# Kernel tuning notes

Measured on AMD Instinct MI355X. Metric: run time of the kernel, lower is better.

## Reference

```python
import jax, jax.numpy as jnp
import numpy as np

B, F_IN, F_OUT, D, K = 32, 64, 64, 512, 64


def setup_inputs() -> dict:
    key = jax.random.key(0)
    k1, k2, k3 = jax.random.split(key, 3)
    x = jax.random.normal(k1, (B, F_IN, D), dtype=jnp.float32)
    # Evaluated monomial-word operators: K matrices of size D x D
    word_ops = jax.random.normal(k2, (K, D, D), dtype=jnp.float32)
    # nn.init.uniform_ -> U[0,1)
    coeff = jax.random.uniform(k3, (F_OUT, F_IN, K), dtype=jnp.float32)
    return {"x": x, "word_ops": word_ops, "coeff": coeff}


def reference(x, word_ops, coeff):
    # Per sample in the torch code:
    #   evals[i, d, k] = (X @ W_k)[i, d] = sum_e X[i, e] * W[k, e, d]
    #   res = tensordot(coeff, evals, ([1, 2], [0, 2]))  -> [F_out, D]
    # Fully batched fused contraction (replaces the Python loop over batch):
    # evals: [B, F_in, D, K]
    evals = jnp.einsum('bie,ked->bidk', x, word_ops)
    # out: [B, F_out, D]
    out = jnp.einsum('oik,bidk->bod', coeff, evals)
    return out
```

## Files before the change

kernel.cpp:

```cpp
#include <hip/hip_runtime.h>


#define KK 32768

typedef __attribute__((ext_vector_type(8))) short bf16x8;
typedef __attribute__((ext_vector_type(4))) float f32x4;

__device__ __forceinline__ unsigned short f2bf(float f) {
  unsigned int u = __float_as_uint(f);
  return (unsigned short)((u + 0x7FFFu + ((u >> 16) & 1u)) >> 16);
}

__device__ __forceinline__ void gld16(void* lds, const void* g) {
  __builtin_amdgcn_global_load_lds((const __attribute__((address_space(1))) void*)g,
                                   (__attribute__((address_space(3))) void*)lds,
                                   16, 0, 0);
}

__global__ __launch_bounds__(256) void convW(const float* __restrict__ W,
                                             unsigned short* __restrict__ WbT) {
  __shared__ float tile[64][65];
  int bx = blockIdx.x;
  int k = bx >> 6, et = (bx >> 3) & 7, dt = bx & 7;
  int t = threadIdx.x;
  const float* src = W + ((size_t)k * 512 + (size_t)et * 64) * 512 + dt * 64;
  int rr = t >> 6, cc = t & 63;
#pragma unroll
  for (int p = 0; p < 16; p++) {
    int e = p * 4 + rr;
    tile[e][cc] = src[(size_t)e * 512 + cc];
  }
  __syncthreads();
  int dl = t >> 4, eg = t & 15;
#pragma unroll
  for (int p = 0; p < 4; p++) {
    int d = p * 16 + dl;
    ushort4 v;
    v.x = f2bf(tile[eg * 4 + 0][d]);
    v.y = f2bf(tile[eg * 4 + 1][d]);
    v.z = f2bf(tile[eg * 4 + 2][d]);
    v.w = f2bf(tile[eg * 4 + 3][d]);
    *(ushort4*)(WbT + (size_t)(dt * 64 + d) * KK + k * 512 + et * 64 + eg * 4) = v;
  }
}

__global__ __launch_bounds__(256) void convX(const float* __restrict__ x,
                                             unsigned short* __restrict__ xT) {
  int tid = blockIdx.x * 256 + threadIdx.x;
  int b = tid >> 15;
  int r = tid & 32767;
  int e = r >> 6, i = r & 63;
  xT[tid] = f2bf(x[((size_t)(b * 64 + i)) * 512 + e]);
}

__global__ __launch_bounds__(256) void convC(const float* __restrict__ c,
                                             unsigned short* __restrict__ cb) {
  int tid = blockIdx.x * 256 + threadIdx.x;
  int k = tid >> 12, r = tid & 4095;
  cb[tid] = f2bf(c[(size_t)r * 64 + k]);
}

__global__ __launch_bounds__(256) void tkern(const unsigned short* __restrict__ xT,
                                             const unsigned short* __restrict__ cb,
                                             unsigned short* __restrict__ Tb) {
  __shared__ unsigned short xe[128 * 88];
  __shared__ unsigned short ck[64 * 64];
  __shared__ unsigned short ot[64 * 136];
  int bx = blockIdx.x;
  int b = bx >> 8, k = (bx >> 2) & 63, eq = bx & 3;
  int t = threadIdx.x;
  {
    const bf16x8* src = (const bf16x8*)(xT + (size_t)b * 32768 + (size_t)eq * 128 * 64);
#pragma unroll
    for (int j = 0; j < 4; j++) {
      int idx = j * 256 + t, e = idx >> 3, c = idx & 7;
      *(bf16x8*)(xe + e * 88 + c * 8) = src[idx];
    }
    const bf16x8* cs = (const bf16x8*)(cb + (size_t)k * 4096);
#pragma unroll
    for (int j = 0; j < 2; j++) *(bf16x8*)(ck + (j * 256 + t) * 8) = cs[j * 256 + t];
  }
  __syncthreads();
  int wid = t >> 6, lane = t & 63, q = lane >> 4, l16 = lane & 15;
  int o0 = wid * 16;
  bf16x8 a0 = *(const bf16x8*)(ck + (o0 + l16) * 64 + q * 8);
  bf16x8 a1 = *(const bf16x8*)(ck + (o0 + l16) * 64 + q * 8 + 32);
#pragma unroll
  for (int et = 0; et < 8; et++) {
    int e = et * 16 + l16;
    bf16x8 b0 = *(const bf16x8*)(xe + e * 88 + q * 8);
    bf16x8 b1 = *(const bf16x8*)(xe + e * 88 + q * 8 + 32);
    f32x4 acc = {0.f, 0.f, 0.f, 0.f};
    acc = __builtin_amdgcn_mfma_f32_16x16x32_bf16(a0, b0, acc, 0, 0, 0);
    acc = __builtin_amdgcn_mfma_f32_16x16x32_bf16(a1, b1, acc, 0, 0, 0);
#pragma unroll
    for (int r2 = 0; r2 < 4; r2++)
      ot[(o0 + q * 4 + r2) * 136 + et * 16 + l16] = f2bf(acc[r2]);
  }
  __syncthreads();
  size_t base = ((size_t)(b * 64)) * KK + k * 512 + eq * 128;
#pragma unroll
  for (int j = 0; j < 4; j++) {
    int idx = j * 256 + t, o = idx >> 4, c = idx & 15;
    *(bf16x8*)(Tb + base + (size_t)o * KK + c * 8) = *(const bf16x8*)(ot + o * 136 + c * 8);
  }
}

__global__ __launch_bounds__(256, 4) void gemm_kern(const unsigned short* __restrict__ A,
                                                    const unsigned short* __restrict__ Bt,
                                                    float* __restrict__ out) {
  __shared__ unsigned short As[128 * 64];
  __shared__ unsigned short Bs[128 * 64];
  int bx = blockIdx.x;
  int ks = bx & 15, nt = (bx >> 4) & 3, mt = bx >> 6;
  int m0 = mt * 128, n0 = nt * 128, k0 = ks * 2048;
  int t = threadIdx.x;
  int wid = t >> 6, lane = t & 63, q = lane >> 4, l16 = lane & 15;
  int wm = (wid & 1) * 64, wn = (wid >> 1) * 64;
  f32x4 acc[4][4] = {};
  int srow = t >> 3;
  int cg = (t & 7) ^ (srow & 7);
  const char* gabase = (const char*)(A + (size_t)m0 * KK + k0) + (size_t)srow * 65536 + cg * 16;
  const char* gbbase = (const char*)(Bt + (size_t)n0 * KK + k0) + (size_t)srow * 65536 + cg * 16;
  int sw0 = q ^ (l16 & 7);
  int sw1 = (4 | q) ^ (l16 & 7);
#pragma unroll 1
  for (int kc = 0; kc < 2048; kc += 64) {
    const char* ga = gabase + (size_t)kc * 2;
    const char* gb = gbbase + (size_t)kc * 2;
#pragma unroll
    for (int j = 0; j < 4; j++) {
      gld16((char*)As + (j * 256 + t) * 16, ga + (size_t)j * 32 * 65536);
      gld16((char*)Bs + (j * 256 + t) * 16, gb + (size_t)j * 32 * 65536);
    }
    __syncthreads();
#pragma unroll
    for (int ks2 = 0; ks2 < 2; ks2++) {
      int slot = ks2 ? sw1 : sw0;
      bf16x8 af[4], bfr[4];
#pragma unroll
      for (int fr = 0; fr < 4; fr++)
        af[fr] = *(const bf16x8*)(As + (wm + fr * 16 + l16) * 64 + slot * 8);
#pragma unroll
      for (int fc = 0; fc < 4; fc++)
        bfr[fc] = *(const bf16x8*)(Bs + (wn + fc * 16 + l16) * 64 + slot * 8);
#pragma unroll
      for (int fr = 0; fr < 4; fr++)
#pragma unroll
        for (int fc = 0; fc < 4; fc++)
          acc[fr][fc] = __builtin_amdgcn_mfma_f32_16x16x32_bf16(af[fr], bfr[fc], acc[fr][fc], 0, 0, 0);
    }
    __syncthreads();
  }
#pragma unroll
  for (int fr = 0; fr < 4; fr++)
#pragma unroll
    for (int fc = 0; fc < 4; fc++)
#pragma unroll
      for (int r = 0; r < 4; r++)
        atomicAdd(&out[(size_t)(m0 + wm + fr * 16 + q * 4 + r) * 512 + n0 + wn + fc * 16 + l16],
                  acc[fr][fc][r]);
}

__global__ __launch_bounds__(256) void fallback_kern(const float* __restrict__ x,
                                                     const float* __restrict__ W,
                                                     const float* __restrict__ coeff,
                                                     float* __restrict__ out) {
  __shared__ float ev[64][129];
  int b = blockIdx.x >> 6, k = blockIdx.x & 63;
  int t = threadIdx.x, dl = t & 127, half = t >> 7;
  const float* xb = x + (size_t)b * 64 * 512;
  const float* Wk = W + (size_t)k * 512 * 512;
  for (int dc = 0; dc < 4; dc++) {
    int d = dc * 128 + dl;
    for (int i = half * 32; i < half * 32 + 32; i++) {
      float acc = 0.f;
      const float* xr = xb + (size_t)i * 512;
#pragma unroll 4
      for (int e = 0; e < 512; e++) acc += xr[e] * Wk[(size_t)e * 512 + d];
      ev[i][dl] = acc;
    }
    __syncthreads();
    for (int o = half * 32; o < half * 32 + 32; o++) {
      float s = 0.f;
#pragma unroll 8
      for (int i = 0; i < 64; i++) s += coeff[((size_t)o * 64 + i) * 64 + k] * ev[i][dl];
      atomicAdd(&out[((size_t)(b * 64 + o)) * 512 + d], s);
    }
    __syncthreads();
  }
}

extern "C" void kernel_launch(void* const* d_in, const int* in_sizes, int n_in,
                              void* d_out, int out_size, void* d_ws, size_t ws_size,
                              hipStream_t stream) {
  const float* x = (const float*)d_in[0];
  const float* W = (const float*)d_in[1];
  const float* coeff = (const float*)d_in[2];
  float* out = (float*)d_out;
  const size_t OFF_XT = 33554432;
  const size_t OFF_CB = OFF_XT + 2097152;
  const size_t OFF_TB = OFF_CB + 524288;
  const size_t NEED = OFF_TB + 134217728;

  hipMemsetAsync(d_out, 0, (size_t)out_size * sizeof(float), stream);
  if (ws_size >= NEED) {
    unsigned short* WbT = (unsigned short*)d_ws;
    unsigned short* xT  = (unsigned short*)((char*)d_ws + OFF_XT);
    unsigned short* cb  = (unsigned short*)((char*)d_ws + OFF_CB);
    unsigned short* Tb  = (unsigned short*)((char*)d_ws + OFF_TB);
    convW<<<4096, 256, 0, stream>>>(W, WbT);
    convX<<<4096, 256, 0, stream>>>(x, xT);
    convC<<<1024, 256, 0, stream>>>(coeff, cb);
    tkern<<<8192, 256, 0, stream>>>(xT, cb, Tb);
    gemm_kern<<<1024, 256, 0, stream>>>(Tb, WbT, out);
  } else {
    fallback_kern<<<2048, 256, 0, stream>>>(x, W, coeff, out);
  }
}
```

Measured before the change: 251.9 us.

## Retile GEMM with double-buffered LDS, enlarge tkern tiles, coalesce conversion kernels

The main GEMM moves to 256x128 tiles with a K-step of 32 and double-buffered LDS loads via global_load_lds. The next chunk is prefetched while the current one runs on MFMA, which aims to overlap memory with compute and halve the number of blocks doing atomics. tkern now computes a 64x256 tile per block using async LDS loads with XOR swizzling, so it reuses the coefficient fragments across more MFMAs. convX and convC become LDS-transposed, coalesced kernels. The costs are higher register pressure (occupancy bound of 2) and more LDS per block.

```diff
diff --git a/kernel.cpp b/kernel.cpp
--- a/kernel.cpp
+++ b/kernel.cpp
@@ -46,120 +46,178 @@
 
 __global__ __launch_bounds__(256) void convX(const float* __restrict__ x,
                                              unsigned short* __restrict__ xT) {
-  int tid = blockIdx.x * 256 + threadIdx.x;
-  int b = tid >> 15;
-  int r = tid & 32767;
-  int e = r >> 6, i = r & 63;
-  xT[tid] = f2bf(x[((size_t)(b * 64 + i)) * 512 + e]);
+  __shared__ unsigned short lds[64 * 130];
+  int bx = blockIdx.x;
+  int b = bx >> 2, ec = bx & 3;
+  int t = threadIdx.x;
+  const float* src = x + (size_t)b * 32768 + ec * 128;
+#pragma unroll
+  for (int j = 0; j < 32; j++) {
+    int idx = j * 256 + t;
+    int i = idx >> 7, e = idx & 127;
+    lds[i * 130 + e] = f2bf(src[(size_t)i * 512 + e]);
+  }
+  __syncthreads();
+  unsigned short* dst = xT + (size_t)b * 32768 + ec * 128 * 64;
+#pragma unroll
+  for (int j = 0; j < 32; j++) {
+    int idx = j * 256 + t;
+    int e = idx >> 6, i = idx & 63;
+    dst[idx] = lds[i * 130 + e];
+  }
 }
 
 __global__ __launch_bounds__(256) void convC(const float* __restrict__ c,
                                              unsigned short* __restrict__ cb) {
-  int tid = blockIdx.x * 256 + threadIdx.x;
-  int k = tid >> 12, r = tid & 4095;
-  cb[tid] = f2bf(c[(size_t)r * 64 + k]);
-}
-
-__global__ __launch_bounds__(256) void tkern(const unsigned short* __restrict__ xT,
-                                             const unsigned short* __restrict__ cb,
-                                             unsigned short* __restrict__ Tb) {
-  __shared__ unsigned short xe[128 * 88];
-  __shared__ unsigned short ck[64 * 64];
-  __shared__ unsigned short ot[64 * 136];
-  int bx = blockIdx.x;
-  int b = bx >> 8, k = (bx >> 2) & 63, eq = bx & 3;
-  int t = threadIdx.x;
+  __shared__ unsigned short lds[64 * 66];
+  int rb = blockIdx.x;
+  int t = threadIdx.x;
+  const float* src = c + (size_t)rb * 4096;
+#pragma unroll
+  for (int j = 0; j < 16; j++) {
+    int idx = j * 256 + t;
+    int r = idx >> 6, k = idx & 63;
+    lds[r * 66 + k] = f2bf(src[idx]);
+  }
+  __syncthreads();
+#pragma unroll
+  for (int j = 0; j < 16; j++) {
+    int idx = j * 256 + t;
+    int k = idx >> 6, r = idx & 63;
+    cb[(size_t)k * 4096 + rb * 64 + r] = lds[r * 66 + k];
+  }
+}
+
+__global__ __launch_bounds__(256, 2) void tkern(const unsigned short* __restrict__ xT,
+                                                const unsigned short* __restrict__ cb,
+                                                unsigned short* __restrict__ Tb) {
+  __shared__ char smem[40960];
+  unsigned short* xe = (unsigned short*)smem;
+  unsigned short* ck = (unsigned short*)(smem + 32768);
+  unsigned short* ot = (unsigned short*)smem;
+  int bx = blockIdx.x;
+  int eh = bx & 1, k = (bx >> 1) & 63, b = bx >> 7;
+  int t = threadIdx.x;
+  int srow = t >> 3, slot = t & 7;
+  int cg = slot ^ (srow & 7);
   {
-    const bf16x8* src = (const bf16x8*)(xT + (size_t)b * 32768 + (size_t)eq * 128 * 64);
-#pragma unroll
-    for (int j = 0; j < 4; j++) {
-      int idx = j * 256 + t, e = idx >> 3, c = idx & 7;
-      *(bf16x8*)(xe + e * 88 + c * 8) = src[idx];
-    }
-    const bf16x8* cs = (const bf16x8*)(cb + (size_t)k * 4096);
-#pragma unroll
-    for (int j = 0; j < 2; j++) *(bf16x8*)(ck + (j * 256 + t) * 8) = cs[j * 256 + t];
+    const unsigned short* gx = xT + (size_t)b * 32768 + (size_t)eh * 16384 + srow * 64 + cg * 8;
+#pragma unroll
+    for (int j = 0; j < 8; j++)
+      gld16((char*)xe + (j * 256 + t) * 16, gx + (size_t)j * 2048);
+    const unsigned short* gc = cb + (size_t)k * 4096 + srow * 64 + cg * 8;
+#pragma unroll
+    for (int j = 0; j < 2; j++)
+      gld16((char*)ck + (j * 256 + t) * 16, gc + (size_t)j * 2048);
   }
   __syncthreads();
   int wid = t >> 6, lane = t & 63, q = lane >> 4, l16 = lane & 15;
-  int o0 = wid * 16;
-  bf16x8 a0 = *(const bf16x8*)(ck + (o0 + l16) * 64 + q * 8);
-  bf16x8 a1 = *(const bf16x8*)(ck + (o0 + l16) * 64 + q * 8 + 32);
-#pragma unroll
-  for (int et = 0; et < 8; et++) {
-    int e = et * 16 + l16;
-    bf16x8 b0 = *(const bf16x8*)(xe + e * 88 + q * 8);
-    bf16x8 b1 = *(const bf16x8*)(xe + e * 88 + q * 8 + 32);
-    f32x4 acc = {0.f, 0.f, 0.f, 0.f};
-    acc = __builtin_amdgcn_mfma_f32_16x16x32_bf16(a0, b0, acc, 0, 0, 0);
-    acc = __builtin_amdgcn_mfma_f32_16x16x32_bf16(a1, b1, acc, 0, 0, 0);
-#pragma unroll
-    for (int r2 = 0; r2 < 4; r2++)
-      ot[(o0 + q * 4 + r2) * 136 + et * 16 + l16] = f2bf(acc[r2]);
-  }
-  __syncthreads();
-  size_t base = ((size_t)(b * 64)) * KK + k * 512 + eq * 128;
-#pragma unroll
-  for (int j = 0; j < 4; j++) {
-    int idx = j * 256 + t, o = idx >> 4, c = idx & 15;
-    *(bf16x8*)(Tb + base + (size_t)o * KK + c * 8) = *(const bf16x8*)(ot + o * 136 + c * 8);
-  }
-}
-
-__global__ __launch_bounds__(256, 4) void gemm_kern(const unsigned short* __restrict__ A,
+  f32x4 acc[4][4] = {};
+  bf16x8 af[4][2];
+#pragma unroll
+  for (int mf = 0; mf < 4; mf++)
+#pragma unroll
+    for (int ks2 = 0; ks2 < 2; ks2++) {
+      int row = mf * 16 + l16;
+      int s2 = (ks2 * 4 + q) ^ (row & 7);
+      af[mf][ks2] = *(const bf16x8*)(ck + row * 64 + s2 * 8);
+    }
+#pragma unroll
+  for (int nf = 0; nf < 4; nf++) {
+    int e = wid * 64 + nf * 16 + l16;
+#pragma unroll
+    for (int ks2 = 0; ks2 < 2; ks2++) {
+      int s2 = (ks2 * 4 + q) ^ (e & 7);
+      bf16x8 bfr = *(const bf16x8*)(xe + e * 64 + s2 * 8);
+#pragma unroll
+      for (int mf = 0; mf < 4; mf++)
+        acc[mf][nf] = __builtin_amdgcn_mfma_f32_16x16x32_bf16(af[mf][ks2], bfr, acc[mf][nf], 0, 0, 0);
+    }
+  }
+  __syncthreads();
+#pragma unroll
+  for (int mf = 0; mf < 4; mf++)
+#pragma unroll
+    for (int nf = 0; nf < 4; nf++)
+#pragma unroll
+      for (int r = 0; r < 4; r++) {
+        int o = mf * 16 + q * 4 + r;
+        int e = wid * 64 + nf * 16 + l16;
+        ot[o * 260 + e] = f2bf(acc[mf][nf][r]);
+      }
+  __syncthreads();
+  unsigned short* gdst = Tb + (size_t)(b * 64) * KK + (size_t)k * 512 + (size_t)eh * 256;
+#pragma unroll
+  for (int j = 0; j < 16; j++) {
+    int idx = j * 256 + t;
+    int o = idx >> 6, c = idx & 63;
+    *(ushort4*)(gdst + (size_t)o * KK + c * 4) = *(const ushort4*)(ot + o * 260 + c * 4);
+  }
+}
+
+__global__ __launch_bounds__(256, 2) void gemm_kern(const unsigned short* __restrict__ A,
                                                     const unsigned short* __restrict__ Bt,
                                                     float* __restrict__ out) {
-  __shared__ unsigned short As[128 * 64];
-  __shared__ unsigned short Bs[128 * 64];
-  int bx = blockIdx.x;
-  int ks = bx & 15, nt = (bx >> 4) & 3, mt = bx >> 6;
-  int m0 = mt * 128, n0 = nt * 128, k0 = ks * 2048;
+  __shared__ unsigned short As[2][256 * 32];
+  __shared__ unsigned short Bs[2][128 * 32];
+  int bx = blockIdx.x;
+  int nt = bx & 3, mt = (bx >> 2) & 7, ks = bx >> 5;
+  int m0 = mt * 256, n0 = nt * 128;
+  size_t k0 = (size_t)ks * 2048;
   int t = threadIdx.x;
   int wid = t >> 6, lane = t & 63, q = lane >> 4, l16 = lane & 15;
-  int wm = (wid & 1) * 64, wn = (wid >> 1) * 64;
-  f32x4 acc[4][4] = {};
-  int srow = t >> 3;
-  int cg = (t & 7) ^ (srow & 7);
-  const char* gabase = (const char*)(A + (size_t)m0 * KK + k0) + (size_t)srow * 65536 + cg * 16;
-  const char* gbbase = (const char*)(Bt + (size_t)n0 * KK + k0) + (size_t)srow * 65536 + cg * 16;
-  int sw0 = q ^ (l16 & 7);
-  int sw1 = (4 | q) ^ (l16 & 7);
+  int wm = (wid & 1) * 128, wn = (wid >> 1) * 64;
+  f32x4 acc[8][4] = {};
+  int srow = t >> 2;
+  int cg = (t & 3) ^ (srow & 3);
+  const unsigned short* ga = A + (size_t)(m0 + srow) * KK + k0 + cg * 8;
+  const unsigned short* gb = Bt + (size_t)(n0 + srow) * KK + k0 + cg * 8;
+  int sA = q ^ (l16 & 3);
 #pragma unroll 1
-  for (int kc = 0; kc < 2048; kc += 64) {
-    const char* ga = gabase + (size_t)kc * 2;
-    const char* gb = gbbase + (size_t)kc * 2;
-#pragma unroll
-    for (int j = 0; j < 4; j++) {
-      gld16((char*)As + (j * 256 + t) * 16, ga + (size_t)j * 32 * 65536);
-      gld16((char*)Bs + (j * 256 + t) * 16, gb + (size_t)j * 32 * 65536);
-    }
+  for (int it = 0; it < 64; it++) {
+    int cur = it & 1;
+    if (it == 0) {
+#pragma unroll
+      for (int j = 0; j < 4; j++)
+        gld16((char*)As[0] + (j * 256 + t) * 16, ga + (size_t)(j * 64) * KK);
+#pragma unroll
+      for (int j = 0; j < 2; j++)
+        gld16((char*)Bs[0] + (j * 256 + t) * 16, gb + (size_t)(j * 64) * KK);
+      __syncthreads();
+    }
+    if (it < 63) {
+      size_t ko = (size_t)(it + 1) * 32;
+#pragma unroll
+      for (int j = 0; j < 4; j++)
+        gld16((char*)As[cur ^ 1] + (j * 256 + t) * 16, ga + (size_t)(j * 64) * KK + ko);
+#pragma unroll
+      for (int j = 0; j < 2; j++)
+        gld16((char*)Bs[cur ^ 1] + (j * 256 + t) * 16, gb + (size_t)(j * 64) * KK + ko);
+    }
+    const unsigned short* as = As[cur];
+    const unsigned short* bs = Bs[cur];
+    bf16x8 af[8], bfr[4];
+#pragma unroll
+    for (int mf = 0; mf < 8; mf++)
+      af[mf] = *(const bf16x8*)(as + (wm + mf * 16 + l16) * 32 + sA * 8);
+#pragma unroll
+    for (int nf = 0; nf < 4; nf++)
+      bfr[nf] = *(const bf16x8*)(bs + (wn + nf * 16 + l16) * 32 + sA * 8);
+#pragma unroll
+    for (int mf = 0; mf < 8; mf++)
+#pragma unroll
+      for (int nf = 0; nf < 4; nf++)
+        acc[mf][nf] = __builtin_amdgcn_mfma_f32_16x16x32_bf16(af[mf], bfr[nf], acc[mf][nf], 0, 0, 0);
     __syncthreads();
-#pragma unroll
-    for (int ks2 = 0; ks2 < 2; ks2++) {
-      int slot = ks2 ? sw1 : sw0;
-      bf16x8 af[4], bfr[4];
-#pragma unroll
-      for (int fr = 0; fr < 4; fr++)
-        af[fr] = *(const bf16x8*)(As + (wm + fr * 16 + l16) * 64 + slot * 8);
-#pragma unroll
-      for (int fc = 0; fc < 4; fc++)
-        bfr[fc] = *(const bf16x8*)(Bs + (wn + fc * 16 + l16) * 64 + slot * 8);
-#pragma unroll
-      for (int fr = 0; fr < 4; fr++)
-#pragma unroll
-        for (int fc = 0; fc < 4; fc++)
-          acc[fr][fc] = __builtin_amdgcn_mfma_f32_16x16x32_bf16(af[fr], bfr[fc], acc[fr][fc], 0, 0, 0);
-    }
-    __syncthreads();
-  }
-#pragma unroll
-  for (int fr = 0; fr < 4; fr++)
-#pragma unroll
-    for (int fc = 0; fc < 4; fc++)
+  }
+#pragma unroll
+  for (int mf = 0; mf < 8; mf++)
+#pragma unroll
+    for (int nf = 0; nf < 4; nf++)
 #pragma unroll
       for (int r = 0; r < 4; r++)
-        atomicAdd(&out[(size_t)(m0 + wm + fr * 16 + q * 4 + r) * 512 + n0 + wn + fc * 16 + l16],
-                  acc[fr][fc][r]);
+        atomicAdd(&out[(size_t)(m0 + wm + mf * 16 + q * 4 + r) * 512 + n0 + wn + nf * 16 + l16],
+                  acc[mf][nf][r]);
 }
 
 __global__ __launch_bounds__(256) void fallback_kern(const float* __restrict__ x,
@@ -209,11 +267,11 @@
     unsigned short* xT  = (unsigned short*)((char*)d_ws + OFF_XT);
     unsigned short* cb  = (unsigned short*)((char*)d_ws + OFF_CB);
     unsigned short* Tb  = (unsigned short*)((char*)d_ws + OFF_TB);
+    convX<<<128, 256, 0, stream>>>(x, xT);
+    convC<<<64, 256, 0, stream>>>(coeff, cb);
     convW<<<4096, 256, 0, stream>>>(W, WbT);
-    convX<<<4096, 256, 0, stream>>>(x, xT);
-    convC<<<1024, 256, 0, stream>>>(coeff, cb);
-    tkern<<<8192, 256, 0, stream>>>(xT, cb, Tb);
-    gemm_kern<<<1024, 256, 0, stream>>>(Tb, WbT, out);
+    tkern<<<4096, 256, 0, stream>>>(xT, cb, Tb);
+    gemm_kern<<<512, 256, 0, stream>>>(Tb, WbT, out);
   } else {
     fallback_kern<<<2048, 256, 0, stream>>>(x, W, coeff, out);
   }
```

New measurement: 321.3 us. +27.5%, slower.
